# Kernel optimization log

Hardware: AMD Instinct MI355X
Metric: run time of the kernel (lower is better)

The kernel has to match this reference:

```python
import jax, jax.numpy as jnp
import numpy as np

B, CIN, COUT, K, H, W = 8, 256, 256, 3, 128, 128


def setup_inputs() -> dict:
    key = jax.random.key(0)
    k1, k2, k3 = jax.random.split(key, 3)
    return {
        "input_vector": jax.random.normal(k1, (B, CIN, H, W), dtype=jnp.float32),
        "style_vector": jax.random.normal(k2, (B, CIN), dtype=jnp.float32),
        "weight": jax.random.normal(k3, (COUT, CIN, K, K), dtype=jnp.float32),
    }


def reference(input_vector, style_vector, weight):
    b, cin, h, w = input_vector.shape
    cout, _, k, _ = weight.shape
    # per-sample modulated weights: (b, O, I, k, k)
    ws = weight[None, :, :, :, :] * style_vector[:, None, :, None, None]
    # NOTE: faithful to source - sum over dims [1,2,3] = (O, I, kh), NOT kw.
    demod = jax.lax.rsqrt(jnp.sum(ws * ws, axis=(1, 2, 3), keepdims=True) + 1e-8)  # (b,1,1,1,k)
    ws = (ws * demod).reshape(b * cout, cin, k, k)
    x = input_vector.reshape(1, b * cin, h, w)
    # get_same_padding(W, k, dilation=1, stride=1) = (k-1)//2
    pad = ((w - 1) * (1 - 1) + 1 * (k - 1)) // 2
    out = jax.lax.conv_general_dilated(
        x, ws,
        window_strides=(1, 1),
        padding=[(pad, pad), (pad, pad)],
        feature_group_count=b,
        dimension_numbers=("NCHW", "OIHW", "NCHW"),
    )
    out = out.reshape(b, cout, h, w)
    return jax.nn.leaky_relu(out, negative_slope=0.2)
```

## Files before the change

### kernel.cpp

```cpp
#include <hip/hip_runtime.h>
#include <hip/hip_bf16.h>

#define B_    8
#define CIN   256
#define COUT  256
#define H_    128
#define W_    128
#define HP    130
#define WP    130

#define OCT   128
#define TROWS 8
#define TCOLS 32
#define XROWS 10
#define XCOLS 34
#define XCH   1360
#define XCHP  1536
#define NSTEP 24
#define KHS   ((size_t)3 * COUT * CIN)

using bfrag = __attribute__((ext_vector_type(8))) short;
using f32x4 = __attribute__((ext_vector_type(4))) float;

#define ASM_VMCNT(n) asm volatile("s_waitcnt vmcnt(" #n ")" ::: "memory")
#define ASM_LGKM0()  asm volatile("s_waitcnt lgkmcnt(0)" ::: "memory")

__device__ __forceinline__ float leaky(float v) {
    return v >= 0.f ? v : 0.2f * v;
}

__device__ __forceinline__ unsigned short to_bf16(float v) {
    __hip_bfloat16 h = __float2bfloat16(v);
    return *(unsigned short*)&h;
}

__global__ void compute_S_kernel(const float* __restrict__ weight, float* __restrict__ S) {
    const int i = blockIdx.x;
    const int t = threadIdx.x;
    const float* wp = weight + ((size_t)t * CIN + i) * 9;
    float s0 = 0.f, s1 = 0.f, s2 = 0.f;
#pragma unroll
    for (int kh = 0; kh < 3; ++kh) {
        float a = wp[kh * 3 + 0], b = wp[kh * 3 + 1], c = wp[kh * 3 + 2];
        s0 = fmaf(a, a, s0); s1 = fmaf(b, b, s1); s2 = fmaf(c, c, s2);
    }
    __shared__ float red[3][256];
    red[0][t] = s0; red[1][t] = s1; red[2][t] = s2;
    __syncthreads();
    for (int off = 128; off > 0; off >>= 1) {
        if (t < off) {
            red[0][t] += red[0][t + off];
            red[1][t] += red[1][t + off];
            red[2][t] += red[2][t + off];
        }
        __syncthreads();
    }
    if (t == 0) {
        S[i * 3 + 0] = red[0][0];
        S[i * 3 + 1] = red[1][0];
        S[i * 3 + 2] = red[2][0];
    }
}

__global__ void compute_demod_kernel(const float* __restrict__ style,
                                     const float* __restrict__ S,
                                     float* __restrict__ demod) {
    const int b = blockIdx.x;
    const int t = threadIdx.x;
    float sv = style[b * CIN + t];
    float sv2 = sv * sv;
    float s0 = sv2 * S[t * 3 + 0];
    float s1 = sv2 * S[t * 3 + 1];
    float s2 = sv2 * S[t * 3 + 2];
    __shared__ float red[3][256];
    red[0][t] = s0; red[1][t] = s1; red[2][t] = s2;
    __syncthreads();
    for (int off = 128; off > 0; off >>= 1) {
        if (t < off) {
            red[0][t] += red[0][t + off];
            red[1][t] += red[1][t + off];
            red[2][t] += red[2][t + off];
        }
        __syncthreads();
    }
    if (t == 0) {
        demod[b * 3 + 0] = rsqrtf(red[0][0] + 1e-8f);
        demod[b * 3 + 1] = rsqrtf(red[1][0] + 1e-8f);
        demod[b * 3 + 2] = rsqrtf(red[2][0] + 1e-8f);
    }
}

__global__ void compute_wmodT_kernel(const float* __restrict__ weight,
                                     const float* __restrict__ style,
                                     const float* __restrict__ demod,
                                     unsigned short* __restrict__ wT) {
    const int bx = blockIdx.x;
    const int i  = threadIdx.x;
    const int o  = bx & (COUT - 1);
    const int j  = (bx >> 8) % 9;
    const int b  = bx / (9 * COUT);
    float w = weight[((size_t)o * CIN + i) * 9 + j];
    float m = style[b * CIN + i] * demod[b * 3 + (j % 3)];
    wT[(((size_t)(b * 9 + j) * COUT + o)) * CIN + i] = to_bf16(w * m);
}

__global__ __launch_bounds__(256) void transpose_kernel(const float* __restrict__ x,
                                                        unsigned short* __restrict__ xT) {
    const int bx = blockIdx.x;
    const int wtile = (bx & 3) * 32;
    const int itile = (bx >> 2) * 32;
    const int h = blockIdx.y;
    const int b = blockIdx.z;
    const int t = threadIdx.x;

    __shared__ float lt[32][33];

    {
        const int tw = t & 31, tr = t >> 5;
#pragma unroll
        for (int rr = 0; rr < 4; ++rr) {
            int il = tr + rr * 8;
            lt[il][tw] = x[(((size_t)b * CIN + itile + il) * H_ + h) * W_ + wtile + tw];
        }
    }
    __syncthreads();
    {
        const int il = t & 31, wr = t >> 5;
#pragma unroll
        for (int rr = 0; rr < 4; ++rr) {
            int wl = wr + rr * 8;
            xT[(((size_t)b * HP + (h + 1)) * WP + (wtile + wl + 1)) * CIN + itile + il] =
                to_bf16(lt[il][wl]);
        }
    }
}

__global__ void zero_border_kernel(unsigned short* __restrict__ xT) {
    const int b = blockIdx.x;
    const int r = blockIdx.y;
    const int t = threadIdx.x;
    int npix, base, stride;
    if (r == 0)      { npix = WP;  base = 0;                 stride = 1;  }
    else if (r == 1) { npix = WP;  base = (HP - 1) * WP;     stride = 1;  }
    else if (r == 2) { npix = 128; base = WP;                stride = WP; }
    else             { npix = 128; base = WP + (WP - 1);     stride = WP; }
    for (int idx = t; idx < npix * 32; idx += 256) {
        int p = idx >> 5, q = idx & 31;
        size_t off = ((size_t)b * HP * WP + base + (size_t)p * stride) * CIN;
        *(int4*)((unsigned short*)xT + off + q * 8) = (int4){0, 0, 0, 0};
    }
}

__global__ __launch_bounds__(256, 2) void conv_mfma_kernel(
    const unsigned short* __restrict__ xT,
    const unsigned short* __restrict__ wT,
    float* __restrict__ out)
{
    const int tid = threadIdx.x;
    const int lin = blockIdx.x;
    const int b    = lin & 7;
    const int rest = lin >> 3;
    const int oc0  = (rest & 1) * OCT;
    const int w0   = ((rest >> 1) & 3) * TCOLS;
    const int h0   = (rest >> 3) * TROWS;

    const int wid   = tid >> 6;
    const int lane  = tid & 63;
    const int wm    = wid >> 1;
    const int cw    = wid & 1;
    const int l15   = lane & 15;
    const int khalf = lane >> 4;

    __shared__ unsigned short lds_a[2][3 * OCT * 32];
    __shared__ unsigned short lds_x[XCHP * 8];

    const unsigned short* xb = xT + ((size_t)(b * HP + h0) * WP + w0) * CIN;
    const unsigned short* wb = wT + ((size_t)(b * 9) * COUT + oc0) * CIN;

    int offA[6];
#pragma unroll
    for (int j = 0; j < 6; ++j) {
        int c    = (wid * 6 + j) * 64 + lane;
        int slot = c & 3;
        int o    = (c >> 2) & 127;
        int kw   = c >> 9;
        offA[j] = (kw * COUT + o) * CIN + ((slot ^ ((o >> 1) & 3)) << 3);
    }
    int offX[6];
#pragma unroll
    for (int j = 0; j < 6; ++j) {
        int g  = (wid * 6 + j) * 64 + lane;
        int gg = g < XCH ? g : 0;
        int pix = gg >> 2, slot = gg & 3;
        int row = pix / XCOLS, col = pix - row * XCOLS;
        offX[j] = (row * WP + col) * CIN + ((slot ^ ((col >> 1) & 3)) << 3);
    }

    f32x4 acc[4][8];
#pragma unroll
    for (int m = 0; m < 4; ++m)
#pragma unroll
        for (int n = 0; n < 8; ++n) acc[m][n] = (f32x4){0.f, 0.f, 0.f, 0.f};

    auto stage_A = [&](unsigned short* dst, const unsigned short* wsrc) {
#pragma unroll
        for (int j = 0; j < 6; ++j) {
            __builtin_amdgcn_global_load_lds(
                (const __attribute__((address_space(1))) void*)(wsrc + offA[j]),
                (__attribute__((address_space(3))) void*)(dst + (wid * 6 + j) * 512),
                16, 0, 0);
        }
    };
    auto stage_X = [&](int i0) {
#pragma unroll
        for (int j = 0; j < 6; ++j) {
            __builtin_amdgcn_global_load_lds(
                (const __attribute__((address_space(1))) void*)(xb + offX[j] + i0),
                (__attribute__((address_space(3))) void*)(lds_x + (wid * 6 + j) * 512),
                16, 0, 0);
        }
    };

    auto compute = [&](int kh, const unsigned short* ab) {
        __builtin_amdgcn_s_setprio(1);
#pragma unroll
        for (int kw = 0; kw < 3; ++kw) {
            bfrag aF[4];
#pragma unroll
            for (int m = 0; m < 4; ++m) {
                int oc = wm * 64 + m * 16 + l15;
                aF[m] = *(const bfrag*)&ab[(kw * OCT + oc) * 32
                          + ((khalf ^ ((oc >> 1) & 3)) << 3)];
            }
#pragma unroll
            for (int n = 0; n < 8; ++n) {
                int row = n + kh;
                int col = cw * 16 + l15 + kw;
                bfrag bF = *(const bfrag*)&lds_x[(row * XCOLS + col) * 32
                             + ((khalf ^ ((col >> 1) & 3)) << 3)];
#pragma unroll
                for (int m = 0; m < 4; ++m)
                    acc[m][n] = __builtin_amdgcn_mfma_f32_16x16x32_bf16(
                        aF[m], bF, acc[m][n], 0, 0, 0);
            }
        }
        __builtin_amdgcn_s_setprio(0);
    };

    stage_X(0);
    stage_A(lds_a[0], wb);
    ASM_VMCNT(0);
    __builtin_amdgcn_s_barrier();
    __builtin_amdgcn_sched_barrier(0);

#pragma unroll 1
    for (int s = 0; s < NSTEP; ++s) {
        const int c  = s / 3;
        const int kh = s - 3 * c;
        unsigned short* acur = lds_a[s & 1];
        unsigned short* anxt = lds_a[(s + 1) & 1];

        if (s < NSTEP - 1) {
            const int sn = s + 1;
            const int cn2 = sn / 3;
            const int khn = sn - 3 * cn2;
            stage_A(anxt, wb + (size_t)khn * KHS + cn2 * 32);
        }
        if (kh == 0) {
            ASM_VMCNT(6);
            __builtin_amdgcn_s_barrier();
            __builtin_amdgcn_sched_barrier(0);
        }
        compute(kh, acur);
        ASM_LGKM0();
        ASM_VMCNT(0);
        __builtin_amdgcn_s_barrier();
        __builtin_amdgcn_sched_barrier(0);
        if (kh == 2 && s < NSTEP - 1)
            stage_X((c + 1) * 32);
    }

#pragma unroll
    for (int m = 0; m < 4; ++m) {
#pragma unroll
        for (int n = 0; n < 8; ++n) {
            int h = h0 + n;
            int w = w0 + cw * 16 + l15;
#pragma unroll
            for (int r = 0; r < 4; ++r) {
                int oc = oc0 + wm * 64 + m * 16 + khalf * 4 + r;
                out[(((size_t)b * COUT + oc) * H_ + h) * W_ + w] = leaky(acc[m][n][r]);
            }
        }
    }
}

extern "C" void kernel_launch(void* const* d_in, const int* in_sizes, int n_in,
                              void* d_out, int out_size, void* d_ws, size_t ws_size,
                              hipStream_t stream) {
    const float* x      = (const float*)d_in[0];
    const float* style  = (const float*)d_in[1];
    const float* weight = (const float*)d_in[2];
    float* out = (float*)d_out;

    float* S     = (float*)d_ws;
    float* demod = (float*)((char*)d_ws + 4096);
    unsigned short* wT = (unsigned short*)((char*)d_ws + 8192);
    unsigned short* xT = (unsigned short*)((char*)d_ws + 9445376);

    compute_S_kernel<<<CIN, 256, 0, stream>>>(weight, S);
    compute_demod_kernel<<<B_, 256, 0, stream>>>(style, S, demod);
    compute_wmodT_kernel<<<B_ * 9 * COUT, 256, 0, stream>>>(weight, style, demod, wT);
    transpose_kernel<<<dim3(32, H_, B_), 256, 0, stream>>>(x, xT);
    zero_border_kernel<<<dim3(B_, 4), 256, 0, stream>>>(xT);

    conv_mfma_kernel<<<dim3(1024), 256, 0, stream>>>(xT, wT, out);
}
```

Before: 188.7 us.

## Software-pipeline LDS fragment loads against MFMAs and unroll kh phases

Rewrites the inner compute loop so A and B fragment reads from LDS are issued two steps ahead in a rotating register buffer and interleaved with MFMA groups via sched_group_barrier. The step loop is unrolled per kh into three phases, with precomputed LDS offsets and one barrier pair per phase, so the weight prefetch for the next phase overlaps compute without a full vmcnt(0) drain each step. The aim is to hide LDS latency and cut synchronization stalls. It adds register pressure, and the pipelining depends on the vmcnt counting staying correct, including the wraparound prefetch on the final chunk.

```diff
diff --git a/kernel.cpp b/kernel.cpp
--- a/kernel.cpp
+++ b/kernel.cpp
@@ -16,7 +16,6 @@
 #define XCOLS 34
 #define XCH   1360
 #define XCHP  1536
-#define NSTEP 24
 #define KHS   ((size_t)3 * COUT * CIN)
 
 using bfrag = __attribute__((ext_vector_type(8))) short;
@@ -196,6 +195,14 @@
         offX[j] = (row * WP + col) * CIN + ((slot ^ ((col >> 1) & 3)) << 3);
     }
 
+    const int aoff = (wm * 64 + l15) * 32 + ((khalf ^ ((l15 >> 1) & 3)) << 3);
+    int boff[3];
+#pragma unroll
+    for (int kw = 0; kw < 3; ++kw) {
+        int col = cw * 16 + l15 + kw;
+        boff[kw] = col * 32 + ((khalf ^ ((col >> 1) & 3)) << 3);
+    }
+
     f32x4 acc[4][8];
 #pragma unroll
     for (int m = 0; m < 4; ++m)
@@ -222,63 +229,75 @@
     };
 
     auto compute = [&](int kh, const unsigned short* ab) {
+        const unsigned short* ap = ab + aoff;
+        const unsigned short* bp[3];
+#pragma unroll
+        for (int kw = 0; kw < 3; ++kw)
+            bp[kw] = lds_x + (size_t)kh * XCOLS * 32 + boff[kw];
+
+        bfrag aF[2][4];
+        bfrag bs[3];
+#pragma unroll
+        for (int m = 0; m < 4; ++m)
+            aF[0][m] = *(const bfrag*)(ap + (size_t)m * 16 * 32);
+        bs[0] = *(const bfrag*)(bp[0]);
+        bs[1] = *(const bfrag*)(bp[0] + (size_t)XCOLS * 32);
+        __builtin_amdgcn_sched_group_barrier(0x100, 6, 0);
+
         __builtin_amdgcn_s_setprio(1);
 #pragma unroll
-        for (int kw = 0; kw < 3; ++kw) {
-            bfrag aF[4];
-#pragma unroll
-            for (int m = 0; m < 4; ++m) {
-                int oc = wm * 64 + m * 16 + l15;
-                aF[m] = *(const bfrag*)&ab[(kw * OCT + oc) * 32
-                          + ((khalf ^ ((oc >> 1) & 3)) << 3)];
+        for (int g = 0; g < 24; ++g) {
+            const int kw = g >> 3, n = g & 7;
+            int nr = 0;
+            if (g <= 21) {
+                const int k2 = g + 2, n2 = k2 & 7, kw2 = k2 >> 3;
+                bs[k2 % 3] = *(const bfrag*)(bp[kw2] + (size_t)n2 * XCOLS * 32);
+                ++nr;
             }
-#pragma unroll
-            for (int n = 0; n < 8; ++n) {
-                int row = n + kh;
-                int col = cw * 16 + l15 + kw;
-                bfrag bF = *(const bfrag*)&lds_x[(row * XCOLS + col) * 32
-                             + ((khalf ^ ((col >> 1) & 3)) << 3)];
-#pragma unroll
-                for (int m = 0; m < 4; ++m)
-                    acc[m][n] = __builtin_amdgcn_mfma_f32_16x16x32_bf16(
-                        aF[m], bF, acc[m][n], 0, 0, 0);
+            if (n >= 1 && n <= 4 && kw < 2) {
+                const int mj = n - 1;
+                aF[(kw + 1) & 1][mj] =
+                    *(const bfrag*)(ap + ((size_t)(kw + 1) * 128 + mj * 16) * 32);
+                ++nr;
             }
+            if (nr == 1) __builtin_amdgcn_sched_group_barrier(0x100, 1, 0);
+            if (nr == 2) __builtin_amdgcn_sched_group_barrier(0x100, 2, 0);
+#pragma unroll
+            for (int m = 0; m < 4; ++m)
+                acc[m][n] = __builtin_amdgcn_mfma_f32_16x16x32_bf16(
+                    aF[kw & 1][m], bs[g % 3], acc[m][n], 0, 0, 0);
+            __builtin_amdgcn_sched_group_barrier(0x8, 4, 0);
         }
         __builtin_amdgcn_s_setprio(0);
     };
 
     stage_X(0);
     stage_A(lds_a[0], wb);
+
+#define PHASE(KH, CUR, NXT, PRE_OFF)                                  \
+    stage_A((NXT), wb + (PRE_OFF));                                   \
+    ASM_VMCNT(6);                                                     \
+    __builtin_amdgcn_s_barrier();                                     \
+    __builtin_amdgcn_sched_barrier(0);                                \
+    compute((KH), (CUR));                                             \
+    ASM_LGKM0();                                                      \
+    __builtin_amdgcn_s_barrier();                                     \
+    __builtin_amdgcn_sched_barrier(0);
+
+#pragma unroll 1
+    for (int c = 0; c < 8; ++c) {
+        unsigned short* pa = lds_a[c & 1];
+        unsigned short* pb = lds_a[(c & 1) ^ 1];
+        const size_t i0  = (size_t)c * 32;
+        const size_t i0n = (size_t)((c + 1) & 7) * 32;
+
+        PHASE(0, pa, pb, KHS + i0)
+        PHASE(1, pb, pa, 2 * KHS + i0)
+        PHASE(2, pa, pb, i0n)
+        if (c < 7) stage_X((int)i0n);
+    }
+#undef PHASE
     ASM_VMCNT(0);
-    __builtin_amdgcn_s_barrier();
-    __builtin_amdgcn_sched_barrier(0);
-
-#pragma unroll 1
-    for (int s = 0; s < NSTEP; ++s) {
-        const int c  = s / 3;
-        const int kh = s - 3 * c;
-        unsigned short* acur = lds_a[s & 1];
-        unsigned short* anxt = lds_a[(s + 1) & 1];
-
-        if (s < NSTEP - 1) {
-            const int sn = s + 1;
-            const int cn2 = sn / 3;
-            const int khn = sn - 3 * cn2;
-            stage_A(anxt, wb + (size_t)khn * KHS + cn2 * 32);
-        }
-        if (kh == 0) {
-            ASM_VMCNT(6);
-            __builtin_amdgcn_s_barrier();
-            __builtin_amdgcn_sched_barrier(0);
-        }
-        compute(kh, acur);
-        ASM_LGKM0();
-        ASM_VMCNT(0);
-        __builtin_amdgcn_s_barrier();
-        __builtin_amdgcn_sched_barrier(0);
-        if (kh == 2 && s < NSTEP - 1)
-            stage_X((c + 1) * 32);
-    }
 
 #pragma unroll
     for (int m = 0; m < 4; ++m) {
```

Measured after the change: 184.7 us. 2.1% less time.
